# Kernel tuning notes

Measured on AMD Instinct MI355X. Metric: run time of the kernel, lower is better.

The kernel has to match this reference:

```python
import jax, jax.numpy as jnp
import numpy as np

N_NODES = 50000
N_EDGES = 640000
D_FEAT = 128
NUM_RELS = 8
EPS = 0.0  # init_eps=0, learn_eps=False -> constant buffer


def setup_inputs() -> dict:
    key = jax.random.key(0)
    k_feat, k_w, k_et, k_src, k_dst = jax.random.split(key, 5)
    feat = jax.random.normal(k_feat, (N_NODES, D_FEAT), dtype=jnp.float32)
    # TypedLinear weight: one [in_feat, out_feat] matrix per relation
    W = jax.random.normal(k_w, (NUM_RELS, D_FEAT, D_FEAT), dtype=jnp.float32) * 0.05
    etypes = jax.random.randint(k_et, (N_EDGES,), 0, NUM_RELS, dtype=jnp.int32)
    src = jax.random.randint(k_src, (N_EDGES,), 0, N_NODES, dtype=jnp.int32)
    dst = jax.random.randint(k_dst, (N_EDGES,), 0, N_NODES, dtype=jnp.int32)
    return {"feat": feat, "W": W, "etypes": etypes, "src": src, "dst": dst}


def reference(feat, W, etypes, src, dst):
    # feat: [N, d]; W: [R, d, d]; etypes/src/dst: [E]
    n_nodes = feat.shape[0]
    num_rels = W.shape[0]
    x = feat[src]  # gather source features, [E, d]
    # TypedLinear: m_e = x_e @ W[etype_e]. Loop over the small fixed relation
    # set (grouped-GEMM form) instead of materializing [E, d, d] weights.
    m = jnp.zeros_like(x)
    for r in range(num_rels):
        mask = (etypes == r)[:, None]
        m = m + jnp.where(mask, x, 0.0) @ W[r]
    # sum aggregation over destination nodes (update_all with fn.sum)
    neigh = jax.ops.segment_sum(m, dst, num_segments=n_nodes)  # [N, d]
    # GIN update: (1 + eps) * h + sum of messages; apply_func/activation are None
    return (1.0 + EPS) * feat + neigh
```

## Files before the change

kernel.cpp:

```cpp
#include <hip/hip_runtime.h>
#include <hip/hip_bf16.h>
#include <stdint.h>

#define D 128
#define CAP 48
#define OVFCAP 65536

using bf16x8 = __attribute__((ext_vector_type(8))) short;
using f32x4  = __attribute__((ext_vector_type(4))) float;
using u32x4  = __attribute__((ext_vector_type(4))) unsigned int;

__device__ __forceinline__ unsigned short f2bf(float f) {
    unsigned u = __float_as_uint(f);
    u = (u + 0x7fffu + ((u >> 16) & 1u)) >> 16;
    return (unsigned short)u;
}
__device__ __forceinline__ float bf2f(unsigned short h) {
    return __uint_as_float(((unsigned)h) << 16);
}

__device__ __forceinline__ bf16x8 cvt8(float4 a, float4 b) {
    union { bf16x8 v; __hip_bfloat162 h[4]; } u;
    u.h[0] = __float22bfloat162_rn(make_float2(a.x, a.y));
    u.h[1] = __float22bfloat162_rn(make_float2(a.z, a.w));
    u.h[2] = __float22bfloat162_rn(make_float2(b.x, b.y));
    u.h[3] = __float22bfloat162_rn(make_float2(b.z, b.w));
    return u.v;
}

__device__ __forceinline__ u32x4 pack2(f32x4 x, f32x4 y) {
    union { u32x4 u; __hip_bfloat162 h[4]; } o;
    o.h[0] = __float22bfloat162_rn(make_float2(x[0], x[1]));
    o.h[1] = __float22bfloat162_rn(make_float2(x[2], x[3]));
    o.h[2] = __float22bfloat162_rn(make_float2(y[0], y[1]));
    o.h[3] = __float22bfloat162_rn(make_float2(y[2], y[3]));
    return o.u;
}

__global__ __launch_bounds__(256) void prep3_kernel(
    const float* __restrict__ feat, unsigned short* __restrict__ featb,
    const float* __restrict__ W, unsigned short* __restrict__ Wt,
    int* __restrict__ deg ,
    int N, int fcTotal , int wtTotal)
{
    int zBlocks  = (N + 1 + 255) >> 8;
    int fcBlocks = (fcTotal + 255) >> 8;
    int b = blockIdx.x;
    if (b < zBlocks) {
        int i = b * 256 + threadIdx.x;
        if (i <= N) deg[i] = 0;
    } else if (b < zBlocks + fcBlocks) {
        int i = (b - zBlocks) * 256 + threadIdx.x;
        if (i < fcTotal) {
            const float4* p = (const float4*)feat + (size_t)i * 2;
            *(bf16x8*)(featb + (size_t)i * 8) = cvt8(p[0], p[1]);
        }
    } else {
        int idx = (b - zBlocks - fcBlocks) * 256 + threadIdx.x;
        if (idx < wtTotal) {
            int r = idx >> 14;
            int rem = idx & 16383;
            int k = rem >> 7, c = rem & 127;
            Wt[(r << 14) + (c << 7) + k] = f2bf(W[idx]);
        }
    }
}

__global__ __launch_bounds__(256) void fused3_kernel(
    const unsigned short* __restrict__ featb, const unsigned short* __restrict__ Wt,
    unsigned short* __restrict__ H,
    const int* __restrict__ dst, const int* __restrict__ et,
    const int* __restrict__ src,
    int* __restrict__ deg, unsigned int* __restrict__ slots,
    int* __restrict__ ovf,
    int N, int NBX, int tBlocks, int cntBlocks, int E)
{
    __shared__ __align__(16) unsigned short sW[128 * 128];
    const int b = blockIdx.x;
    const long long total = (long long)tBlocks + cntBlocks;

    long long cb = ((long long)b * cntBlocks) / total;
    bool isCount = (((long long)(b + 1) * cntBlocks) / total) > cb;

    if (isCount) {
        int e = (int)cb * 256 + threadIdx.x;
        if (e < E) {
            int d = dst[e];
            unsigned key = ((unsigned)et[e] * (unsigned)N + (unsigned)src[e]) << 8;
            int ord = atomicAdd(&deg[d], 1);
            if (ord < CAP) {
                __builtin_nontemporal_store(key, &slots[(size_t)d * CAP + ord]);
            } else {
                int o = atomicAdd(&deg[N], 1);
                if (o < OVFCAP) ovf[o] = e;
            }
        }
        return;
    }

    const int tIdx = b - (int)cb;
    const int rel = tIdx / NBX;
    const int bx  = tIdx - rel * NBX;
    const int tid  = threadIdx.x;
    const int wave = tid >> 6, lane = tid & 63;
    const int q    = lane >> 4, mlo = lane & 15;

    {
        const ulonglong2* wsrc = (const ulonglong2*)(Wt + ((size_t)rel << 14));
        #pragma unroll
        for (int i = 0; i < 8; ++i) {
            int idx = tid + 256 * i;
            int row = idx >> 4, ch = idx & 15;
            ulonglong2 v = wsrc[idx];
            *(ulonglong2*)&sW[row * 128 + ((ch ^ (row & 15)) * 8)] = v;
        }
    }

    const int nb = bx * 128 + wave * 32;
    bf16x8 bfr[2][4];
    int nodeg[2];
    #pragma unroll
    for (int g = 0; g < 2; ++g) {
        int node = nb + g * 16 + mlo;
        nodeg[g] = node;
        int ld = node < N ? node : N - 1;
        const unsigned short* fp = featb + (size_t)ld * D + q * 8;
        #pragma unroll
        for (int ks = 0; ks < 4; ++ks)
            bfr[g][ks] = *(const bf16x8*)(fp + ks * 32);
    }
    __syncthreads();

    const size_t Hb = (size_t)rel * N * D;
    unsigned short* hp0 = H + Hb + (size_t)nodeg[0] * D + q * 8;
    unsigned short* hp1 = H + Hb + (size_t)nodeg[1] * D + q * 8;

    #pragma unroll
    for (int j = 0; j < 4; ++j) {
        bf16x8 af0[4], af1[4];
        const int row0 = (2 * j) * 16 + mlo, row1 = row0 + 16;
        #pragma unroll
        for (int ks = 0; ks < 4; ++ks) {
            af0[ks] = *(const bf16x8*)&sW[row0 * 128 + (((ks * 4 + q) ^ mlo) * 8)];
            af1[ks] = *(const bf16x8*)&sW[row1 * 128 + (((ks * 4 + q) ^ mlo) * 8)];
        }
        #pragma unroll
        for (int g = 0; g < 2; ++g) {
            f32x4 a = {0.f,0.f,0.f,0.f}, c = {0.f,0.f,0.f,0.f};
            #pragma unroll
            for (int ks = 0; ks < 4; ++ks) {
                a = __builtin_amdgcn_mfma_f32_16x16x32_bf16(af0[ks], bfr[g][ks], a, 0, 0, 0);
                c = __builtin_amdgcn_mfma_f32_16x16x32_bf16(af1[ks], bfr[g][ks], c, 0, 0, 0);
            }
            if (nodeg[g] < N)
                __builtin_nontemporal_store(pack2(a, c),
                    (u32x4*)((g ? hp1 : hp0) + j * 32));
        }
    }
}

__global__ __launch_bounds__(256) void k_gather6(
    const char* __restrict__ Hc, const unsigned int* __restrict__ slots,
    const int* __restrict__ deg, const float* __restrict__ feat,
    float* __restrict__ out, int N)
{
    int n = blockIdx.x * 4 + (threadIdx.x >> 6);
    if (n >= N) return;
    int lane = threadIdx.x & 63;
    int h = lane >> 5, l5 = lane & 31;

    float2 acc0 = {0.f, 0.f}, acc1 = {0.f, 0.f};

    int dg = deg[n];
    dg = __builtin_amdgcn_readfirstlane(dg);
    int capped = dg < CAP ? dg : CAP;
    if (capped > 0) {
        unsigned ep = slots[(size_t)n * CAP + (lane < capped ? lane : capped - 1)];
        for (int done = 0; done < capped; done += 32) {
            unsigned long long a[16];
            #pragma unroll
            for (int u = 0; u < 16; ++u) {
                int eidx = done + 2 * u + h;
                int cl = eidx < capped ? eidx : capped - 1;
                unsigned p = __shfl(ep, cl);
                a[u] = *(const unsigned long long*)(Hc + p + l5 * 8);
            }
            #pragma unroll
            for (int u = 0; u < 16; ++u) {
                bool v = (done + 2 * u + h) < capped;
                unsigned lo = (unsigned)a[u], hi = (unsigned)(a[u] >> 32);
                acc0.x += v ? bf2f((unsigned short)(lo & 0xffffu)) : 0.f;
                acc0.y += v ? bf2f((unsigned short)(lo >> 16)) : 0.f;
                acc1.x += v ? bf2f((unsigned short)(hi & 0xffffu)) : 0.f;
                acc1.y += v ? bf2f((unsigned short)(hi >> 16)) : 0.f;
            }
        }
    }
    acc0.x += __shfl(acc0.x, lane ^ 32);
    acc0.y += __shfl(acc0.y, lane ^ 32);
    acc1.x += __shfl(acc1.x, lane ^ 32);
    acc1.y += __shfl(acc1.y, lane ^ 32);
    if (h == 0) {
        int f4 = 8 * (l5 >> 3) + 4 * (l5 & 1) + ((l5 >> 1) & 3);
        float4 fv = ((const float4*)feat)[(size_t)n * 32 + f4];
        float4 o;
        o.x = fv.x + acc0.x; o.y = fv.y + acc0.y;
        o.z = fv.z + acc1.x; o.w = fv.w + acc1.y;
        ((float4*)out)[(size_t)n * 32 + f4] = o;
    }
}

__global__ __launch_bounds__(256) void k_ovf(
    const char* __restrict__ Hc, const int* __restrict__ ovf,
    const int* __restrict__ deg ,
    const int* __restrict__ dst, const int* __restrict__ et,
    const int* __restrict__ src, float* __restrict__ out, int N)
{
    int cnt = deg[N];
    if (cnt > OVFCAP) cnt = OVFCAP;
    int wid = (blockIdx.x * 256 + threadIdx.x) >> 6;
    int nw = (gridDim.x * 256) >> 6;
    int lane = threadIdx.x & 63;
    const int jj = lane >> 4, qq = (lane >> 2) & 3, pp = lane & 3;
    const int f = 16 * jj + 8 * (pp >> 1) + 2 * qq + (pp & 1);
    for (int i = wid; i < cnt; i += nw) {
        int e = ovf[i];
        int d = dst[e];
        unsigned key = ((unsigned)et[e] * (unsigned)N + (unsigned)src[e]) << 8;
        unsigned a = *(const unsigned*)(Hc + key + lane * 4);
        atomicAdd(out + (size_t)d * D + 2 * f,     bf2f((unsigned short)(a & 0xffffu)));
        atomicAdd(out + (size_t)d * D + 2 * f + 1, bf2f((unsigned short)(a >> 16)));
    }
}

__global__ __launch_bounds__(256) void init_kernel(
    const float* __restrict__ feat, float* __restrict__ out, int n4)
{
    int i = blockIdx.x * 256 + threadIdx.x;
    if (i < n4) ((float4*)out)[i] = ((const float4*)feat)[i];
}

__global__ __launch_bounds__(128) void edge_matvec_kernel(
    const float* __restrict__ feat, const float* __restrict__ W,
    const int* __restrict__ et, const int* __restrict__ src,
    const int* __restrict__ dst, float* __restrict__ out, int E)
{
    __shared__ float xs[D];
    int e = blockIdx.x;
    int c = threadIdx.x;
    int s = src[e], r = et[e], d = dst[e];
    xs[c] = feat[(size_t)s * D + c];
    __syncthreads();
    const float* Wr = W + (size_t)r * D * D;
    float acc = 0.f;
    #pragma unroll 8
    for (int k = 0; k < D; ++k) acc += xs[k] * Wr[(size_t)k * D + c];
    atomicAdd(out + (size_t)d * D + c, acc);
}

static inline size_t al256(size_t x) { return (x + 255) & ~(size_t)255; }

extern "C" void kernel_launch(void* const* d_in, const int* in_sizes, int n_in,
                              void* d_out, int out_size, void* d_ws, size_t ws_size,
                              hipStream_t stream) {
    const float* feat = (const float*)d_in[0];
    const float* W    = (const float*)d_in[1];
    const int*   et   = (const int*)d_in[2];
    const int*   src  = (const int*)d_in[3];
    const int*   dst  = (const int*)d_in[4];
    float* out = (float*)d_out;

    const int N = in_sizes[0] / D;
    const int R = in_sizes[1] / (D * D);
    const int E = in_sizes[2];

    size_t hB   = al256((size_t)R * N * D * sizeof(unsigned short));
    size_t wtB  = al256((size_t)R * D * D * sizeof(unsigned short));
    size_t degB = al256((size_t)(N + 1) * sizeof(int));
    size_t sltB = al256((size_t)N * CAP * sizeof(unsigned int));
    size_t ovfB = al256((size_t)OVFCAP * sizeof(int));
    size_t fbB  = al256((size_t)N * D * sizeof(unsigned short));
    size_t need = hB + wtB + degB + sltB + ovfB + fbB;

    const bool packable = ((size_t)R * (size_t)N * 256ull <= 0xFFFFFFFFull);

    if (ws_size >= need && packable) {
        char* p = (char*)d_ws;
        unsigned short* H      = (unsigned short*)p;           p += hB;
        unsigned short* Wt     = (unsigned short*)p;           p += wtB;
        int*            deg    = (int*)p;                      p += degB;
        unsigned int*   slots  = (unsigned int*)p;             p += sltB;
        int*            ovf    = (int*)p;                      p += ovfB;
        unsigned short* featb  = (unsigned short*)p;

        int wtTotal = R * D * D;
        int fcTotal = (N * D) / 8;
        int zBlocks  = (N + 1 + 255) / 256;
        int fcBlocks = (fcTotal + 255) / 256;
        int wtBlocks = (wtTotal + 255) / 256;
        int cntBlocks = (E + 255) / 256;

        prep3_kernel<<<zBlocks + fcBlocks + wtBlocks, 256, 0, stream>>>(
            feat, featb, W, Wt, deg, N, fcTotal, wtTotal);

        int NBX = (N + 127) / 128;
        int tBlocks = NBX * R;
        fused3_kernel<<<tBlocks + cntBlocks, 256, 0, stream>>>(
            featb, Wt, H, dst, et, src, deg, slots, ovf,
            N, NBX, tBlocks, cntBlocks, E);

        k_gather6<<<(N + 3) / 4, 256, 0, stream>>>(
            (const char*)H, slots, deg, feat, out, N);

        k_ovf<<<16, 256, 0, stream>>>(
            (const char*)H, ovf, deg, dst, et, src, out, N);
    } else {
        int n4 = (N * D) / 4;
        init_kernel<<<(n4 + 255) / 256, 256, 0, stream>>>(feat, out, n4);
        edge_matvec_kernel<<<E, 128, 0, stream>>>(feat, W, et, src, dst, out, E);
    }
}
```

Baseline: 185.3 us.

## Pad degree counters, batch 4 edges per count thread, drop nontemporal H stores

Spaces each node's degree counter 16 ints (64 bytes) apart so concurrent atomics to different nodes hit separate cache lines. Each counting thread now handles four edges, issuing all loads before its atomics to raise memory-level parallelism, and there are a quarter as many count blocks. The H stores become regular stores so the later gather can find them in cache. In exchange, the degree array becomes 16x larger, which means more zeroing work in prep and a sparser, strided read of degrees in the gather.

```diff
diff --git a/kernel.cpp b/kernel.cpp
--- a/kernel.cpp
+++ b/kernel.cpp
@@ -41,14 +41,14 @@
     const float* __restrict__ feat, unsigned short* __restrict__ featb,
     const float* __restrict__ W, unsigned short* __restrict__ Wt,
     int* __restrict__ deg ,
-    int N, int fcTotal , int wtTotal)
-{
-    int zBlocks  = (N + 1 + 255) >> 8;
+    int N, int fcTotal , int wtTotal, int degTotal)
+{
+    int zBlocks  = (degTotal + 255) >> 8;
     int fcBlocks = (fcTotal + 255) >> 8;
     int b = blockIdx.x;
     if (b < zBlocks) {
         int i = b * 256 + threadIdx.x;
-        if (i <= N) deg[i] = 0;
+        if (i < degTotal) deg[i] = 0;
     } else if (b < zBlocks + fcBlocks) {
         int i = (b - zBlocks) * 256 + threadIdx.x;
         if (i < fcTotal) {
@@ -73,7 +73,7 @@
     const int* __restrict__ src,
     int* __restrict__ deg, unsigned int* __restrict__ slots,
     int* __restrict__ ovf,
-    int N, int NBX, int tBlocks, int cntBlocks, int E)
+    int N, int NBX, int tBlocks, int cntBlocks, int E, int ds)
 {
     __shared__ __align__(16) unsigned short sW[128 * 128];
     const int b = blockIdx.x;
@@ -83,16 +83,29 @@
     bool isCount = (((long long)(b + 1) * cntBlocks) / total) > cb;
 
     if (isCount) {
-        int e = (int)cb * 256 + threadIdx.x;
-        if (e < E) {
-            int d = dst[e];
-            unsigned key = ((unsigned)et[e] * (unsigned)N + (unsigned)src[e]) << 8;
-            int ord = atomicAdd(&deg[d], 1);
-            if (ord < CAP) {
-                __builtin_nontemporal_store(key, &slots[(size_t)d * CAP + ord]);
-            } else {
-                int o = atomicAdd(&deg[N], 1);
-                if (o < OVFCAP) ovf[o] = e;
+        int base = (int)cb * 1024 + threadIdx.x;
+        int dv[4]; unsigned key[4]; int ord[4]; bool v[4];
+        #pragma unroll
+        for (int t = 0; t < 4; ++t) {
+            int e = base + t * 256;
+            v[t] = e < E;
+            int el = v[t] ? e : 0;
+            dv[t]  = dst[el];
+            key[t] = ((unsigned)et[el] * (unsigned)N + (unsigned)src[el]) << 8;
+        }
+        #pragma unroll
+        for (int t = 0; t < 4; ++t)
+            ord[t] = v[t] ? atomicAdd(&deg[(size_t)dv[t] * ds], 1) : CAP;
+        #pragma unroll
+        for (int t = 0; t < 4; ++t) {
+            if (v[t]) {
+                if (ord[t] < CAP) {
+                    __builtin_nontemporal_store(key[t],
+                        &slots[(size_t)dv[t] * CAP + ord[t]]);
+                } else {
+                    int o = atomicAdd(&deg[(size_t)N * ds], 1);
+                    if (o < OVFCAP) ovf[o] = base + t * 256;
+                }
             }
         }
         return;
@@ -153,8 +166,7 @@
                 c = __builtin_amdgcn_mfma_f32_16x16x32_bf16(af1[ks], bfr[g][ks], c, 0, 0, 0);
             }
             if (nodeg[g] < N)
-                __builtin_nontemporal_store(pack2(a, c),
-                    (u32x4*)((g ? hp1 : hp0) + j * 32));
+                *(u32x4*)((g ? hp1 : hp0) + j * 32) = pack2(a, c);
         }
     }
 }
@@ -162,7 +174,7 @@
 __global__ __launch_bounds__(256) void k_gather6(
     const char* __restrict__ Hc, const unsigned int* __restrict__ slots,
     const int* __restrict__ deg, const float* __restrict__ feat,
-    float* __restrict__ out, int N)
+    float* __restrict__ out, int N, int ds)
 {
     int n = blockIdx.x * 4 + (threadIdx.x >> 6);
     if (n >= N) return;
@@ -171,7 +183,7 @@
 
     float2 acc0 = {0.f, 0.f}, acc1 = {0.f, 0.f};
 
-    int dg = deg[n];
+    int dg = deg[(size_t)n * ds];
     dg = __builtin_amdgcn_readfirstlane(dg);
     int capped = dg < CAP ? dg : CAP;
     if (capped > 0) {
@@ -214,9 +226,9 @@
     const char* __restrict__ Hc, const int* __restrict__ ovf,
     const int* __restrict__ deg ,
     const int* __restrict__ dst, const int* __restrict__ et,
-    const int* __restrict__ src, float* __restrict__ out, int N)
-{
-    int cnt = deg[N];
+    const int* __restrict__ src, float* __restrict__ out, int N, int ds)
+{
+    int cnt = deg[(size_t)N * ds];
     if (cnt > OVFCAP) cnt = OVFCAP;
     int wid = (blockIdx.x * 256 + threadIdx.x) >> 6;
     int nw = (gridDim.x * 256) >> 6;
@@ -276,11 +288,18 @@
 
     size_t hB   = al256((size_t)R * N * D * sizeof(unsigned short));
     size_t wtB  = al256((size_t)R * D * D * sizeof(unsigned short));
-    size_t degB = al256((size_t)(N + 1) * sizeof(int));
     size_t sltB = al256((size_t)N * CAP * sizeof(unsigned int));
     size_t ovfB = al256((size_t)OVFCAP * sizeof(int));
     size_t fbB  = al256((size_t)N * D * sizeof(unsigned short));
+
+    int ds = 16;
+    size_t degB = al256(((size_t)N * ds + 1) * sizeof(int));
     size_t need = hB + wtB + degB + sltB + ovfB + fbB;
+    if (ws_size < need) {
+        ds = 1;
+        degB = al256(((size_t)N + 1) * sizeof(int));
+        need = hB + wtB + degB + sltB + ovfB + fbB;
+    }
 
     const bool packable = ((size_t)R * (size_t)N * 256ull <= 0xFFFFFFFFull);
 
@@ -293,27 +312,28 @@
         int*            ovf    = (int*)p;                      p += ovfB;
         unsigned short* featb  = (unsigned short*)p;
 
-        int wtTotal = R * D * D;
-        int fcTotal = (N * D) / 8;
-        int zBlocks  = (N + 1 + 255) / 256;
+        int wtTotal  = R * D * D;
+        int fcTotal  = (N * D) / 8;
+        int degTotal = N * ds + 1;
+        int zBlocks  = (degTotal + 255) / 256;
         int fcBlocks = (fcTotal + 255) / 256;
         int wtBlocks = (wtTotal + 255) / 256;
-        int cntBlocks = (E + 255) / 256;
+        int cntBlocks = (E + 1023) / 1024;
 
         prep3_kernel<<<zBlocks + fcBlocks + wtBlocks, 256, 0, stream>>>(
-            feat, featb, W, Wt, deg, N, fcTotal, wtTotal);
+            feat, featb, W, Wt, deg, N, fcTotal, wtTotal, degTotal);
 
         int NBX = (N + 127) / 128;
         int tBlocks = NBX * R;
         fused3_kernel<<<tBlocks + cntBlocks, 256, 0, stream>>>(
             featb, Wt, H, dst, et, src, deg, slots, ovf,
-            N, NBX, tBlocks, cntBlocks, E);
+            N, NBX, tBlocks, cntBlocks, E, ds);
 
         k_gather6<<<(N + 3) / 4, 256, 0, stream>>>(
-            (const char*)H, slots, deg, feat, out, N);
+            (const char*)H, slots, deg, feat, out, N, ds);
 
         k_ovf<<<16, 256, 0, stream>>>(
-            (const char*)H, ovf, deg, dst, et, src, out, N);
+            (const char*)H, ovf, deg, dst, et, src, out, N, ds);
     } else {
         int n4 = (N * D) / 4;
         init_kernel<<<(n4 + 255) / 256, 256, 0, stream>>>(feat, out, n4);
```

Result: faster. 172.3 us (-7.0%).
